# Kernel optimization log

Hardware: AMD Instinct MI355X
Metric: run time of the kernel (lower is better)

The kernel has to match this reference:

```python
import jax, jax.numpy as jnp
import numpy as np

N_NODES = 50000

def setup_inputs() -> dict:
    key = jax.random.key(0)
    k1, k2, k3, k4, k5 = jax.random.split(key, 5)
    x = jax.random.normal(k1, (50000, 64), dtype=jnp.float32)
    adj_rows = jax.random.randint(k2, (800000,), 0, 50000, dtype=jnp.int32)
    adj_cols = jax.random.randint(k3, (800000,), 0, 50000, dtype=jnp.int32)
    adj_vals = jax.random.uniform(k4, (800000,), dtype=jnp.float32)
    ws = jax.random.uniform(k5, (4,), dtype=jnp.float32)
    return {"x": x, "adj_rows": adj_rows, "adj_cols": adj_cols, "adj_vals": adj_vals, "ws": ws, "idx": 0}

def reference(x, adj_rows, adj_cols, adj_vals, ws, idx):
    # spmm: out[r] = sum_{e: rows[e]==r} vals[e] * x[cols[e]]
    msgs = adj_vals[:, None] * x[adj_cols]              # [E, d]
    spmm = jax.ops.segment_sum(msgs, adj_rows, num_segments=N_NODES)  # [N, d]
    return ws[idx] * spmm
```

## Files before the change

kernel.cpp:

```cpp
#include <hip/hip_runtime.h>

#define N_NODES 50000
#define N_EDGES 800000
#define D 64

#define NBUCK 782
#define CAP   2048
#define SRT_CAP 2048

#define A_EPB 8192
#define A_BLOCKS ((N_EDGES + A_EPB - 1) / A_EPB)
#define A_THREADS 512

#define F_THREADS 512

typedef unsigned short ushort_t;

__global__ __launch_bounds__(1024) void initg_kernel(int* __restrict__ gcur)
{
    int b = threadIdx.x;
    if (b < NBUCK) gcur[b] = b * CAP;
}

__global__ __launch_bounds__(256) void cvt_kernel(
    const float* __restrict__ x, ushort_t* __restrict__ xb)
{
    int i = blockIdx.x * 256 + threadIdx.x;
    float4 v = reinterpret_cast<const float4*>(x)[i];
    ushort4 o;
    unsigned bx;
    bx = __float_as_uint(v.x); o.x = (ushort_t)((bx + 0x7fffu + ((bx >> 16) & 1u)) >> 16);
    bx = __float_as_uint(v.y); o.y = (ushort_t)((bx + 0x7fffu + ((bx >> 16) & 1u)) >> 16);
    bx = __float_as_uint(v.z); o.z = (ushort_t)((bx + 0x7fffu + ((bx >> 16) & 1u)) >> 16);
    bx = __float_as_uint(v.w); o.w = (ushort_t)((bx + 0x7fffu + ((bx >> 16) & 1u)) >> 16);
    reinterpret_cast<ushort4*>(xb)[i] = o;
}

__global__ __launch_bounds__(A_THREADS) void bin_kernel(
    const int* __restrict__ rows, const int* __restrict__ cols,
    const float* __restrict__ vals, int* __restrict__ gcur,
    int2* __restrict__ buckets)
{
    __shared__ int2 rec[A_EPB];
    __shared__ int2 srt[A_EPB];
    __shared__ int cnt[NBUCK];
    __shared__ int lofs[NBUCK];
    __shared__ int lcur[NBUCK];
    __shared__ int bbase[NBUCK];

    const int tid = threadIdx.x;
    const int e0  = blockIdx.x * A_EPB;
    const int n   = min(A_EPB, N_EDGES - e0);

    for (int i = tid; i < NBUCK; i += A_THREADS) cnt[i] = 0;
    __syncthreads();

    for (int i = tid; i < n; i += A_THREADS) {
        int r = rows[e0 + i];
        int c = cols[e0 + i];
        float v = vals[e0 + i];
        rec[i].x = (int)(((unsigned)r << 16) | (unsigned)c);
        rec[i].y = __float_as_int(v);
        atomicAdd(&cnt[r >> 6], 1);
    }
    __syncthreads();

    if (tid < 64) {
        int lane = tid, carry = 0;
        for (int seg = 0; seg < (NBUCK + 63) / 64; ++seg) {
            int j = seg * 64 + lane;
            int v = (j < NBUCK) ? cnt[j] : 0;
            int incl = v;
            for (int off = 1; off < 64; off <<= 1) {
                int u = __shfl_up(incl, off);
                if (lane >= off) incl += u;
            }
            if (j < NBUCK) lofs[j] = carry + incl - v;
            carry += __shfl(incl, 63);
        }
    }
    __syncthreads();

    for (int j = tid; j < NBUCK; j += A_THREADS) {
        int c = cnt[j];
        bbase[j] = c ? atomicAdd(&gcur[j], c) : 0;
        lcur[j]  = lofs[j];
    }
    __syncthreads();

    for (int i = tid; i < n; i += A_THREADS) {
        int2 rv = rec[i];
        int b = ((unsigned)rv.x) >> 22;
        int p = atomicAdd(&lcur[b], 1);
        srt[p] = rv;
    }
    __syncthreads();

    for (int i = tid; i < n; i += A_THREADS) {
        int2 rv = srt[i];
        int b = ((unsigned)rv.x) >> 22;
        buckets[bbase[b] + (i - lofs[b])] = rv;
    }
}

__global__ __launch_bounds__(F_THREADS) void sortgather_kernel(
    const ushort_t* __restrict__ xb, const int2* __restrict__ buckets,
    const int* __restrict__ gcur, const float* __restrict__ ws,
    const int* __restrict__ idx, float* __restrict__ out)
{
    __shared__ int2 srt[SRT_CAP];
    __shared__ int cnt[64];
    __shared__ int lofs[65];
    __shared__ int lcur[64];

    const int b    = blockIdx.x;
    const int tid  = threadIdx.x;
    const int lane = tid & 63;
    const int w    = tid >> 6;
    const int base = b * CAP;
    const int nb   = gcur[b] - base;

    if (tid < 64) cnt[tid] = 0;
    __syncthreads();

    for (int i = tid; i < nb; i += F_THREADS) {
        int rx = buckets[base + i].x;
        atomicAdd(&cnt[(rx >> 16) & 63], 1);
    }
    __syncthreads();

    if (w == 0) {
        int v = cnt[lane];
        int incl = v;
        for (int off = 1; off < 64; off <<= 1) {
            int u = __shfl_up(incl, off);
            if (lane >= off) incl += u;
        }
        lofs[lane] = incl - v;
        if (lane == 63) lofs[64] = incl;
    }
    __syncthreads();
    if (tid < 64) lcur[tid] = lofs[tid];
    __syncthreads();

    for (int i = tid; i < nb; i += F_THREADS) {
        int2 rv = buckets[base + i];
        int p = atomicAdd(&lcur[(rv.x >> 16) & 63], 1);
        srt[p] = rv;
    }
    __syncthreads();

    const float wgt = ws[idx[0]];
    for (int q = 0; q < 8; ++q) {
        const int lr   = w * 8 + q;
        const int seg0 = lofs[lr];
        const int seg1 = lofs[lr + 1];
        float acc0 = 0.f, acc1 = 0.f;
        for (int cb = seg0; cb < seg1; cb += 16) {
            int le = cb + (lane & 15);
            int2 cv = srt[le < seg1 ? le : seg0];
            int ci = cv.x;
            int vi = (le < seg1) ? cv.y : 0;
#pragma unroll
            for (int k = 0; k < 16; ++k) {
                int sx = __builtin_amdgcn_readlane(ci, k);
                int sv = __builtin_amdgcn_readlane(vi, k);
                int c  = sx & 0xffff;
                ushort_t u = xb[(size_t)c * D + lane];
                float xv = __uint_as_float(((unsigned)u) << 16);
                if (k & 1) acc1 += __int_as_float(sv) * xv;
                else       acc0 += __int_as_float(sv) * xv;
            }
        }
        const int row = b * 64 + lr;
        if (row < N_NODES)
            out[(size_t)row * D + lane] = wgt * (acc0 + acc1);
    }
}

extern "C" void kernel_launch(void* const* d_in, const int* in_sizes, int n_in,
                              void* d_out, int out_size, void* d_ws, size_t ws_size,
                              hipStream_t stream) {
    const float* x    = (const float*)d_in[0];
    const int*   rows = (const int*)d_in[1];
    const int*   cols = (const int*)d_in[2];
    const float* vals = (const float*)d_in[3];
    const float* ws   = (const float*)d_in[4];
    const int*   idx  = (const int*)d_in[5];
    float*       out  = (float*)d_out;

    const size_t xb_bytes      = (size_t)N_NODES * D * sizeof(ushort_t);
    const size_t buckets_bytes = (size_t)NBUCK * CAP * sizeof(int2);

    char* wsb = (char*)d_ws;
    ushort_t* xb      = (ushort_t*)wsb;
    int2*     buckets = (int2*)(wsb + xb_bytes);
    int*      gcur    = (int*)(wsb + xb_bytes + buckets_bytes);

    initg_kernel<<<dim3(1), dim3(1024), 0, stream>>>(gcur);

    cvt_kernel<<<dim3(N_NODES * D / 4 / 256), dim3(256), 0, stream>>>(x, xb);

    bin_kernel<<<dim3(A_BLOCKS), dim3(A_THREADS), 0, stream>>>(
        rows, cols, vals, gcur, buckets);

    sortgather_kernel<<<dim3(NBUCK), dim3(F_THREADS), 0, stream>>>(
        xb, buckets, gcur, ws, idx, out);
}
```

Measured before the change: 56.91 us.

## Split gather into feature halves across two blocks, fold init into convert

The sort-gather kernel now launches two blocks per bucket, each covering 32 of the 64 features. Inside a block, the two half-wavefronts handle alternating edges, and their partial sums are combined with a cross-lane shuffle. This doubles the parallelism of the gather phase. The cost is that every bucket's local counting sort runs twice, and the 32-lane bf16 loads are narrower. The separate init kernel is merged into the convert kernel to save a launch, and the bin kernel's edges per block is halved to 4096 so it runs more blocks.

```diff
diff --git a/kernel.cpp b/kernel.cpp
--- a/kernel.cpp
+++ b/kernel.cpp
@@ -8,23 +8,22 @@
 #define CAP   2048
 #define SRT_CAP 2048
 
-#define A_EPB 8192
+#define A_EPB 4096
 #define A_BLOCKS ((N_EDGES + A_EPB - 1) / A_EPB)
 #define A_THREADS 512
 
 #define F_THREADS 512
+#define F_GRID 1568
 
 typedef unsigned short ushort_t;
 
-__global__ __launch_bounds__(1024) void initg_kernel(int* __restrict__ gcur)
+__global__ __launch_bounds__(256) void cvt_kernel(
+    const float* __restrict__ x, ushort_t* __restrict__ xb,
+    int* __restrict__ gcur)
 {
-    int b = threadIdx.x;
-    if (b < NBUCK) gcur[b] = b * CAP;
-}
-
-__global__ __launch_bounds__(256) void cvt_kernel(
-    const float* __restrict__ x, ushort_t* __restrict__ xb)
-{
+    if (blockIdx.x == 0) {
+        for (int j = threadIdx.x; j < NBUCK; j += 256) gcur[j] = j * CAP;
+    }
     int i = blockIdx.x * 256 + threadIdx.x;
     float4 v = reinterpret_cast<const float4*>(x)[i];
     ushort4 o;
@@ -113,9 +112,14 @@
     __shared__ int lofs[65];
     __shared__ int lcur[64];
 
-    const int b    = blockIdx.x;
+    const int blk  = blockIdx.x;
+    const int half = ((blk & 7) >= 4) ? 1 : 0;
+    const int b    = ((blk >> 3) << 2) + (blk & 3);
+    if (b >= NBUCK) return;
+
     const int tid  = threadIdx.x;
     const int lane = tid & 63;
+    const int hl   = lane & 31;
     const int w    = tid >> 6;
     const int base = b * CAP;
     const int nb   = gcur[b] - base;
@@ -151,30 +155,36 @@
     __syncthreads();
 
     const float wgt = ws[idx[0]];
+    const ushort_t* __restrict__ xh = xb + half * 32 + hl;
     for (int q = 0; q < 8; ++q) {
-        const int lr   = w * 8 + q;
-        const int seg0 = lofs[lr];
-        const int seg1 = lofs[lr + 1];
+        const int lr = w * 8 + q;
+        const int s0 = lofs[lr];
+        const int s1 = lofs[lr + 1];
         float acc0 = 0.f, acc1 = 0.f;
-        for (int cb = seg0; cb < seg1; cb += 16) {
-            int le = cb + (lane & 15);
-            int2 cv = srt[le < seg1 ? le : seg0];
+        for (int cb = s0; cb < s1; cb += 32) {
+            int le = cb + hl;
+            int2 cv = srt[le < s1 ? le : s0];
             int ci = cv.x;
-            int vi = (le < seg1) ? cv.y : 0;
+            int vi = (le < s1) ? cv.y : 0;
 #pragma unroll
-            for (int k = 0; k < 16; ++k) {
-                int sx = __builtin_amdgcn_readlane(ci, k);
-                int sv = __builtin_amdgcn_readlane(vi, k);
-                int c  = sx & 0xffff;
-                ushort_t u = xb[(size_t)c * D + lane];
+            for (int p = 0; p < 16; ++p) {
+                int cA = __builtin_amdgcn_readlane(ci, 2 * p);
+                int vA = __builtin_amdgcn_readlane(vi, 2 * p);
+                int cB = __builtin_amdgcn_readlane(ci, 2 * p + 1);
+                int vB = __builtin_amdgcn_readlane(vi, 2 * p + 1);
+                int c = ((lane < 32) ? cA : cB) & 0xffff;
+                int v = (lane < 32) ? vA : vB;
+                ushort_t u = xh[(size_t)c * D];
                 float xv = __uint_as_float(((unsigned)u) << 16);
-                if (k & 1) acc1 += __int_as_float(sv) * xv;
-                else       acc0 += __int_as_float(sv) * xv;
+                if (p & 1) acc1 += __int_as_float(v) * xv;
+                else       acc0 += __int_as_float(v) * xv;
             }
         }
+        float acc = acc0 + acc1;
+        acc += __shfl_xor(acc, 32);
         const int row = b * 64 + lr;
-        if (row < N_NODES)
-            out[(size_t)row * D + lane] = wgt * (acc0 + acc1);
+        if (lane < 32 && row < N_NODES)
+            out[(size_t)row * D + half * 32 + hl] = wgt * acc;
     }
 }
 
@@ -197,13 +207,11 @@
     int2*     buckets = (int2*)(wsb + xb_bytes);
     int*      gcur    = (int*)(wsb + xb_bytes + buckets_bytes);
 
-    initg_kernel<<<dim3(1), dim3(1024), 0, stream>>>(gcur);
-
-    cvt_kernel<<<dim3(N_NODES * D / 4 / 256), dim3(256), 0, stream>>>(x, xb);
+    cvt_kernel<<<dim3(N_NODES * D / 4 / 256), dim3(256), 0, stream>>>(x, xb, gcur);
 
     bin_kernel<<<dim3(A_BLOCKS), dim3(A_THREADS), 0, stream>>>(
         rows, cols, vals, gcur, buckets);
 
-    sortgather_kernel<<<dim3(NBUCK), dim3(F_THREADS), 0, stream>>>(
+    sortgather_kernel<<<dim3(F_GRID), dim3(F_THREADS), 0, stream>>>(
         xb, buckets, gcur, ws, idx, out);
 }
```

Result: slower. 75.14 us (+32.0%).
